# Kernel optimization log

Measured on AMD Instinct MI355X. Metric: run time of the kernel, lower is better.

The kernel has to match this reference:

```python
import jax, jax.numpy as jnp
import numpy as np

EMBED_DIM = 1152
NUM_HEADS = 16
HEAD_DIM = EMBED_DIM // NUM_HEADS  # 72
SCALE = HEAD_DIM ** -0.5


def setup_inputs() -> dict:
    key = jax.random.key(0)
    ks = jax.random.split(key, 5)
    B, S, D = 32, 729, EMBED_DIM
    hidden_states = jax.random.normal(ks[0], (B, S, D), dtype=jnp.float32)
    # fused QKV projection weight/bias (q|k|v concatenated on output dim)
    w_qkv = jax.random.normal(ks[1], (D, 3 * D), dtype=jnp.float32) * (D ** -0.5)
    b_qkv = jax.random.normal(ks[2], (3 * D,), dtype=jnp.float32) * 0.02
    w_out = jax.random.normal(ks[3], (D, D), dtype=jnp.float32) * (D ** -0.5)
    b_out = jax.random.normal(ks[4], (D,), dtype=jnp.float32) * 0.02
    return {"hidden_states": hidden_states, "w_qkv": w_qkv, "b_qkv": b_qkv,
            "w_out": w_out, "b_out": b_out}


def reference(hidden_states, w_qkv, b_qkv, w_out, b_out):
    B, S, D = hidden_states.shape
    qkv = hidden_states @ w_qkv + b_qkv              # [B,S,3D]
    q, k, v = jnp.split(qkv, 3, axis=-1)
    # [B,S,D] -> [B,H,S,hd]
    def to_heads(x):
        return x.reshape(B, S, NUM_HEADS, HEAD_DIM).transpose(0, 2, 1, 3)
    q, k, v = to_heads(q), to_heads(k), to_heads(v)
    scores = jnp.einsum('bhqd,bhkd->bhqk', q, k) * SCALE
    attn = jax.nn.softmax(scores, axis=-1)
    out = jnp.einsum('bhqk,bhkd->bhqd', attn, v)     # [B,H,S,hd]
    out = out.transpose(0, 2, 1, 3).reshape(B, S, D)
    return out @ w_out + b_out
```

## Files before the change

### kernel.cpp

```cpp
#include <hip/hip_runtime.h>
#include <hip/hip_bf16.h>
#include <stdint.h>

typedef unsigned short u16;
typedef __attribute__((ext_vector_type(8))) short bf16x8;
typedef __attribute__((ext_vector_type(4))) float f32x4;
typedef __attribute__((ext_vector_type(4))) unsigned short us4;

#define T_TOK   23328
#define MPAD    23424
#define DMODEL  1152
#define N3      3456
#define NHEAD   16
#define HDIM    72
#define SEQ     729
#define VSTR    736
#define SCALE_F 0.1178511301977579f
#define KVB     64
#define NT      12
#define THR     8.0f

__device__ __forceinline__ u16 f2bf(float f) {
  unsigned u = __builtin_bit_cast(unsigned, f);
  u += 0x7fffu + ((u >> 16) & 1u);
  return (u16)(u >> 16);
}

__device__ __forceinline__ f32x4 mfma16(bf16x8 a, bf16x8 b, f32x4 c) {
  return __builtin_amdgcn_mfma_f32_16x16x32_bf16(a, b, c, 0, 0, 0);
}

#define GL16(g, l)                                                        \
  __builtin_amdgcn_global_load_lds(                                       \
      (const __attribute__((address_space(1))) void*)(g),                 \
      (__attribute__((address_space(3))) void*)(l), 16, 0, 0)


__global__ void k_cvt_hidden(const float* __restrict__ in, u16* __restrict__ out) {
  size_t i4 = ((size_t)blockIdx.x * blockDim.x + threadIdx.x) * 4;
  if (i4 >= (size_t)MPAD * DMODEL) return;
  us4 o;
  if (i4 < (size_t)T_TOK * DMODEL) {
    float4 v = *(const float4*)(in + i4);
    o[0] = f2bf(v.x); o[1] = f2bf(v.y); o[2] = f2bf(v.z); o[3] = f2bf(v.w);
  } else {
    o[0] = 0; o[1] = 0; o[2] = 0; o[3] = 0;
  }
  *(us4*)(out + i4) = o;
}

template <int R, int C>
__global__ void k_transpose(const float* __restrict__ w, u16* __restrict__ wt) {
  size_t i = (size_t)blockIdx.x * blockDim.x + threadIdx.x;
  if (i >= (size_t)R * C) return;
  int n  = (int)(i / R);
  int kk = (int)(i - (size_t)n * R);
  wt[i] = f2bf(w[(size_t)kk * C + n]);
}

template <int EPI, int GX>
__global__ __launch_bounds__(256) void k_gemm(
    const u16* __restrict__ A, const u16* __restrict__ Bt,
    const float* __restrict__ bias,
    u16* __restrict__ qo, u16* __restrict__ ko, u16* __restrict__ vTo,
    float* __restrict__ outp)
{
  __shared__ u16 As[2][4096];
  __shared__ u16 Bs[2][4096];
  const int tid  = threadIdx.x;
  const int wave = tid >> 6;
  const int lane = tid & 63;

  constexpr int nwg = GX * 183;
  constexpr int q8 = nwg >> 3, r8 = nwg & 7;
  const int bid = blockIdx.x;
  const int xcd = bid & 7, idx = bid >> 3;
  const int wgid = (xcd < r8 ? xcd * (q8 + 1) : r8 * (q8 + 1) + (xcd - r8) * q8) + idx;
  const int m0 = (wgid / GX) * 128;
  const int n0 = (wgid % GX) * 128;

  const int wm = (wave >> 1) * 64;
  const int wn = (wave & 1) * 64;

  const int rofs = wave * 16 + (lane >> 2);
  const int cofs = (lane & 3) * 8;
  const u16* gA0 = A  + (size_t)(m0 + rofs) * DMODEL + cofs;
  const u16* gA1 = gA0 + (size_t)64 * DMODEL;
  const u16* gB0 = Bt + (size_t)(n0 + rofs) * DMODEL + cofs;
  const u16* gB1 = gB0 + (size_t)64 * DMODEL;

  const int fr = lane & 15;
  const int fk = (lane >> 4) * 8;

  auto stage = [&](int kt, int b) {
    char* a_ = (char*)As + b * 8192 + wave * 1024;
    char* b_ = (char*)Bs + b * 8192 + wave * 1024;
    GL16(gA0 + kt, a_);
    GL16(gA1 + kt, a_ + 4096);
    GL16(gB0 + kt, b_);
    GL16(gB1 + kt, b_ + 4096);
  };

  f32x4 acc[4][4] = {};

  stage(0, 0);

  int buf = 0;
  for (int kt = 0; kt < DMODEL; kt += 32) {
    if (kt + 32 < DMODEL) {
      stage(kt + 32, buf ^ 1);
      asm volatile("s_waitcnt vmcnt(4)\n\ts_barrier" ::: "memory");
    } else {
      asm volatile("s_waitcnt vmcnt(0)\n\ts_barrier" ::: "memory");
    }
    bf16x8 af[4], bfrag[4];
#pragma unroll
    for (int i = 0; i < 4; ++i)
      af[i] = *(const bf16x8*)&As[buf][(wm + i * 16 + fr) * 32 + fk];
#pragma unroll
    for (int j = 0; j < 4; ++j)
      bfrag[j] = *(const bf16x8*)&Bs[buf][(wn + j * 16 + fr) * 32 + fk];
#pragma unroll
    for (int i = 0; i < 4; ++i)
#pragma unroll
      for (int j = 0; j < 4; ++j)
        acc[i][j] = mfma16(af[i], bfrag[j], acc[i][j]);
    asm volatile("s_barrier" ::: "memory");
    buf ^= 1;
  }

#pragma unroll
  for (int j = 0; j < 4; ++j) {
    const int n = n0 + wn + j * 16 + fr;
    const float bi = bias[n];
    if (EPI == 0) {
      const int which = n / DMODEL;
      const int rr = n - which * DMODEL;
      const int h = rr / HDIM;
      const int d = rr - h * HDIM;
#pragma unroll
      for (int i = 0; i < 4; ++i) {
        const int tr = m0 + wm + i * 16 + (lane >> 4) * 4;
#pragma unroll
        for (int rg = 0; rg < 4; ++rg) {
          const int t = tr + rg;
          if (t < T_TOK) {
            const int bb = t / SEQ;
            const int s  = t - bb * SEQ;
            const int bh = bb * NHEAD + h;
            const float val = acc[i][j][rg] + bi;
            if (which == 0)
              qo[((size_t)bh * SEQ + s) * HDIM + d] = f2bf(val * SCALE_F);
            else if (which == 1)
              ko[((size_t)bh * SEQ + s) * HDIM + d] = f2bf(val);
            else
              vTo[((size_t)bh * HDIM + d) * VSTR + s] = f2bf(val);
          }
        }
      }
    } else {
#pragma unroll
      for (int i = 0; i < 4; ++i) {
        const int tr = m0 + wm + i * 16 + (lane >> 4) * 4;
#pragma unroll
        for (int rg = 0; rg < 4; ++rg) {
          const int t = tr + rg;
          if (t < T_TOK)
            outp[(size_t)t * DMODEL + n] = acc[i][j][rg] + bi;
        }
      }
    }
  }
}


__device__ __forceinline__ void stage_kv(const u16* __restrict__ kb, const u16* __restrict__ vb,
                                         u16* KsB, u16* VsB, int kt, int wv, int lane) {
#pragma unroll
  for (int rdi = 0; rdi < 2; ++rdi) {
    const int c0 = rdi * 256 + wv * 64;
    {
      const int c = c0 + lane;
      const int row = c / 9;
      const int off = (c - row * 9) * 8;
      GL16(kb + (size_t)(kt + row) * HDIM + off, KsB + (size_t)c0 * 8);
    }
    {
      const int c = c0 + lane;
      const int d = c >> 3;
      int off = kt + (((c & 7) ^ (d & 7)) << 3);
      off = off > (VSTR - 8) ? (VSTR - 8) : off;
      GL16(vb + (size_t)d * VSTR + off, VsB + (size_t)c0 * 8);
    }
  }
  if (wv == 0) {
    const int c = 512 + lane;
    const int row = c / 9;
    const int off = (c - row * 9) * 8;
    GL16(kb + (size_t)(kt + row) * HDIM + off, KsB + (size_t)512 * 8);
    const int d = c >> 3;
    int voff = kt + (((c & 7) ^ (d & 7)) << 3);
    voff = voff > (VSTR - 8) ? (VSTR - 8) : voff;
    GL16(vb + (size_t)d * VSTR + voff, VsB + (size_t)512 * 8);
  }
}

__global__ __launch_bounds__(256) void k_attn(
    const u16* __restrict__ q, const u16* __restrict__ k,
    const u16* __restrict__ vT, u16* __restrict__ aout)
{
  __shared__ alignas(16) u16 Ks[2][4640];
  __shared__ alignas(16) u16 Vs[2][5120];
  __shared__ alignas(16) u16 pl[4][16][72];

  const int tid  = threadIdx.x;
  const int wv   = tid >> 6;
  const int lane = tid & 63;
  const int fr = lane & 15;
  const int fg = lane >> 4;
  const int fk = fg * 8;

  const int bh = blockIdx.y;
  const int qbase = blockIdx.x * 64 + wv * 16;

  const u16* qb = q  + (size_t)bh * (SEQ * HDIM);
  const u16* kb = k  + (size_t)bh * (SEQ * HDIM);
  const u16* vb = vT + (size_t)bh * (HDIM * VSTR);

  if (tid < 64) { Vs[0][4608 + tid] = 0x3F80; Vs[1][4608 + tid] = 0x3F80; }
  for (int i = tid; i < 448; i += 256) { Vs[0][4672 + i] = 0; Vs[1][4672 + i] = 0; }
  if (tid < 32) { Ks[0][4608 + tid] = 0; Ks[1][4608 + tid] = 0; }

  const int qrow = qbase + fr;
  bf16x8 qf0 = {}, qf1 = {}, qf2 = {};
  if (qrow < SEQ) {
    const u16* qp = qb + (size_t)qrow * HDIM;
    qf0 = *(const bf16x8*)(qp + fk);
    qf1 = *(const bf16x8*)(qp + 32 + fk);
    if (fg == 0) qf2 = *(const bf16x8*)(qp + 64);
  }

  f32x4 oacc[5] = {};
  float mrun[4] = {-1e30f, -1e30f, -1e30f, -1e30f};

  stage_kv(kb, vb, Ks[0], Vs[0], 0, wv, lane);
  __syncthreads();

  int buf = 0;
  for (int t = 0; t < NT; ++t) {
    const int kt = t * KVB;
    if (t + 1 < NT)
      stage_kv(kb, vb, Ks[buf ^ 1], Vs[buf ^ 1], kt + KVB, wv, lane);

    const char* kB = (const char*)Ks[buf];
    f32x4 sc[4];
#pragma unroll
    for (int hh = 0; hh < 4; ++hh) {
      const char* krow = kB + (hh * 16 + fr) * 144;
      bf16x8 kf0 = *(const bf16x8*)(krow + fg * 16);
      bf16x8 kf1 = *(const bf16x8*)(krow + 64 + fg * 16);
      bf16x8 kf2 = *(const bf16x8*)(krow + 128 + fg * 16);
      f32x4 z = {};
      z = mfma16(qf0, kf0, z);
      z = mfma16(qf1, kf1, z);
      z = mfma16(qf2, kf2, z);
      sc[hh] = z;
    }
    if (kt + KVB > SEQ) {
#pragma unroll
      for (int hh = 0; hh < 4; ++hh)
        if (kt + hh * 16 + fr >= SEQ) {
          sc[hh][0] = -1e30f; sc[hh][1] = -1e30f; sc[hh][2] = -1e30f; sc[hh][3] = -1e30f;
        }
    }

    float tmx[4];
    bool needs = false;
#pragma unroll
    for (int r = 0; r < 4; ++r) {
      tmx[r] = fmaxf(fmaxf(sc[0][r], sc[1][r]), fmaxf(sc[2][r], sc[3][r]));
      needs |= (tmx[r] > mrun[r] + THR);
    }
    if (__any(needs)) {
#pragma unroll
      for (int r = 0; r < 4; ++r) {
        float tm = tmx[r];
        tm = fmaxf(tm, __shfl_xor(tm, 1));
        tm = fmaxf(tm, __shfl_xor(tm, 2));
        tm = fmaxf(tm, __shfl_xor(tm, 4));
        tm = fmaxf(tm, __shfl_xor(tm, 8));
        const float mnew = fmaxf(mrun[r], tm);
        const float resc = __expf(mrun[r] - mnew);
        mrun[r] = mnew;
#pragma unroll
        for (int v = 0; v < 5; ++v) oacc[v][r] *= resc;
      }
    }
#pragma unroll
    for (int r = 0; r < 4; ++r) {
      const int prow = fg * 4 + r;
#pragma unroll
      for (int hh = 0; hh < 4; ++hh)
        pl[wv][prow][hh * 16 + fr] = f2bf(__expf(sc[hh][r] - mrun[r]));
    }

    const bf16x8 pa0 = *(const bf16x8*)&pl[wv][fr][fk];
    const bf16x8 pa1 = *(const bf16x8*)&pl[wv][fr][32 + fk];
    const char* vB = (const char*)Vs[buf];
    const int swz = (fr & 7) << 4;
#pragma unroll
    for (int v = 0; v < 5; ++v) {
      const char* vrow = vB + (size_t)(v * 16 + fr) * 128;
      bf16x8 vf0 = *(const bf16x8*)(vrow + ((fg * 16) ^ swz));
      bf16x8 vf1 = *(const bf16x8*)(vrow + (((4 + fg) * 16) ^ swz));
      oacc[v] = mfma16(pa0, vf0, oacc[v]);
      oacc[v] = mfma16(pa1, vf1, oacc[v]);
    }

    __syncthreads();
    buf ^= 1;
  }

  const int bb = bh >> 4, h = bh & 15;
#pragma unroll
  for (int r = 0; r < 4; ++r) {
    const int row = qbase + fg * 4 + r;
    if (row < SEQ) {
      const float l = __shfl(oacc[4][r], (lane & 48) | 8);
      const float inv = 1.0f / l;
      u16* op = aout + (size_t)(bb * SEQ + row) * DMODEL + h * HDIM;
#pragma unroll
      for (int v = 0; v < 5; ++v) {
        const int d = v * 16 + fr;
        if (d < HDIM) op[d] = f2bf(oacc[v][r] * inv);
      }
    }
  }
}

extern "C" void kernel_launch(void* const* d_in, const int* in_sizes, int n_in,
                              void* d_out, int out_size, void* d_ws, size_t ws_size,
                              hipStream_t stream) {
  (void)in_sizes; (void)n_in; (void)out_size; (void)ws_size;
  const float* hs   = (const float*)d_in[0];
  const float* wqkv = (const float*)d_in[1];
  const float* bqkv = (const float*)d_in[2];
  const float* wout = (const float*)d_in[3];
  const float* bout = (const float*)d_in[4];
  float* out = (float*)d_out;

  u16* hbuf  = (u16*)d_ws;
  u16* wqkvT = hbuf  + (size_t)MPAD * DMODEL;
  u16* woutT = wqkvT + (size_t)N3 * DMODEL;
  u16* qb    = woutT + (size_t)DMODEL * DMODEL;
  u16* kb    = qb    + (size_t)512 * SEQ * HDIM;
  u16* vTb   = kb    + (size_t)512 * SEQ * HDIM;

  k_cvt_hidden<<<(MPAD * DMODEL / 4 + 255) / 256, 256, 0, stream>>>(hs, hbuf);
  k_transpose<DMODEL, N3><<<((size_t)DMODEL * N3 + 255) / 256, 256, 0, stream>>>(wqkv, wqkvT);
  k_transpose<DMODEL, DMODEL><<<((size_t)DMODEL * DMODEL + 255) / 256, 256, 0, stream>>>(wout, woutT);
  k_gemm<0, 27><<<27 * 183, 256, 0, stream>>>(hbuf, wqkvT, bqkv, qb, kb, vTb, nullptr);
  k_attn<<<dim3(12, 512), 256, 0, stream>>>(qb, kb, vTb, hbuf);
  k_gemm<1, 9><<<9 * 183, 256, 0, stream>>>(hbuf, woutT, bout, nullptr, nullptr, nullptr, out);
}
```

Before: 887.7 us.

## Use 256x256 tiled QKV GEMM with 8 waves, swizzled LDS and deeper K-step

Replaces the QKV projection GEMM with a dedicated kernel that uses 256x256 output tiles, 512 threads, 64-wide K steps, XOR-swizzled LDS layout and setprio around MFMA bursts. The weight matrix is padded to 3584 columns and the hidden buffer to 23552 rows so the grid divides evenly. The larger tile raises arithmetic intensity and reduces global traffic for the dominant GEMM. In exchange it raises register and LDS pressure, runs at one block per CU, and spends some work on the padded columns. The output GEMM is split into its own template with the M tile count adjusted.

After: 982.2 us. 10.6% more time.

```diff
diff --git a/kernel.cpp b/kernel.cpp
--- a/kernel.cpp
+++ b/kernel.cpp
@@ -8,9 +8,11 @@
 typedef __attribute__((ext_vector_type(4))) unsigned short us4;
 
 #define T_TOK   23328
-#define MPAD    23424
+#define MPAD    23552
 #define DMODEL  1152
 #define N3      3456
+#define N3P     3584
+#define NKT     18
 #define NHEAD   16
 #define HDIM    72
 #define SEQ     729
@@ -58,96 +60,123 @@
   wt[i] = f2bf(w[(size_t)kk * C + n]);
 }
 
-template <int EPI, int GX>
-__global__ __launch_bounds__(256) void k_gemm(
+template <int RIN, int CIN, int CPAD>
+__global__ void k_transpose_pad(const float* __restrict__ w, u16* __restrict__ wt) {
+  size_t i = (size_t)blockIdx.x * blockDim.x + threadIdx.x;
+  if (i >= (size_t)CPAD * RIN) return;
+  int n  = (int)(i / RIN);
+  int kk = (int)(i - (size_t)n * RIN);
+  wt[i] = (n < CIN) ? f2bf(w[(size_t)kk * CIN + n]) : (u16)0;
+}
+
+__global__ __launch_bounds__(512, 1) void k_gemm_qkv(
     const u16* __restrict__ A, const u16* __restrict__ Bt,
     const float* __restrict__ bias,
-    u16* __restrict__ qo, u16* __restrict__ ko, u16* __restrict__ vTo,
-    float* __restrict__ outp)
+    u16* __restrict__ qo, u16* __restrict__ ko, u16* __restrict__ vTo)
 {
-  __shared__ u16 As[2][4096];
-  __shared__ u16 Bs[2][4096];
+  __shared__ u16 As[2 * 2 * 128 * 64];
+  __shared__ u16 Bs[2 * 2 * 128 * 64];
   const int tid  = threadIdx.x;
-  const int wave = tid >> 6;
+  const int wv   = tid >> 6;
   const int lane = tid & 63;
-
-  constexpr int nwg = GX * 183;
-  constexpr int q8 = nwg >> 3, r8 = nwg & 7;
+  const int wr = wv >> 2;
+  const int wc = wv & 3;
+  const int fr = lane & 15;
+  const int fg = lane >> 4;
+
   const int bid = blockIdx.x;
-  const int xcd = bid & 7, idx = bid >> 3;
-  const int wgid = (xcd < r8 ? xcd * (q8 + 1) : r8 * (q8 + 1) + (xcd - r8) * q8) + idx;
-  const int m0 = (wgid / GX) * 128;
-  const int n0 = (wgid % GX) * 128;
-
-  const int wm = (wave >> 1) * 64;
-  const int wn = (wave & 1) * 64;
-
-  const int rofs = wave * 16 + (lane >> 2);
-  const int cofs = (lane & 3) * 8;
-  const u16* gA0 = A  + (size_t)(m0 + rofs) * DMODEL + cofs;
-  const u16* gA1 = gA0 + (size_t)64 * DMODEL;
-  const u16* gB0 = Bt + (size_t)(n0 + rofs) * DMODEL + cofs;
-  const u16* gB1 = gB0 + (size_t)64 * DMODEL;
-
-  const int fr = lane & 15;
-  const int fk = (lane >> 4) * 8;
-
-  auto stage = [&](int kt, int b) {
-    char* a_ = (char*)As + b * 8192 + wave * 1024;
-    char* b_ = (char*)Bs + b * 8192 + wave * 1024;
-    GL16(gA0 + kt, a_);
-    GL16(gA1 + kt, a_ + 4096);
-    GL16(gB0 + kt, b_);
-    GL16(gB1 + kt, b_ + 4096);
+  const int wgid = (bid & 7) * 161 + (bid >> 3);
+  const int m0 = (wgid / 14) * 256;
+  const int n0 = (wgid % 14) * 256;
+
+  int r_[2], e_[2];
+#pragma unroll
+  for (int j = 0; j < 2; ++j) {
+    const int d  = (j * 512 + wv * 64 + lane) * 16;
+    const int dd = d ^ (((d >> 9) & 1) << 5);
+    r_[j] = dd >> 7;
+    e_[j] = (dd & 127) >> 1;
+  }
+
+  auto stage_tile = [&](int t2) {
+    const int p2 = t2 & 1;
+    char* ab = (char*)As + p2 * 32768;
+    char* bb = (char*)Bs + p2 * 32768;
+    const int kt = t2 * 64;
+#pragma unroll
+    for (int h = 0; h < 2; ++h)
+#pragma unroll
+      for (int j = 0; j < 2; ++j)
+        GL16(A + (size_t)(m0 + h * 128 + r_[j]) * DMODEL + kt + e_[j],
+             ab + h * 16384 + j * 8192 + wv * 1024);
+#pragma unroll
+    for (int h = 0; h < 2; ++h)
+#pragma unroll
+      for (int j = 0; j < 2; ++j)
+        GL16(Bt + (size_t)(n0 + h * 128 + r_[j]) * DMODEL + kt + e_[j],
+             bb + h * 16384 + j * 8192 + wv * 1024);
   };
 
-  f32x4 acc[4][4] = {};
-
-  stage(0, 0);
-
-  int buf = 0;
-  for (int kt = 0; kt < DMODEL; kt += 32) {
-    if (kt + 32 < DMODEL) {
-      stage(kt + 32, buf ^ 1);
-      asm volatile("s_waitcnt vmcnt(4)\n\ts_barrier" ::: "memory");
+  const int aswz = ((fr >> 2) & 1) << 5;
+  const int kof[2] = { (fg * 16) ^ aswz, (64 + fg * 16) ^ aswz };
+  const int arow = fr * 128;
+  const int brow = ((wc & 1) * 64 + fr) * 128;
+
+  f32x4 acc[8][4] = {};
+
+  stage_tile(0);
+  stage_tile(1);
+  asm volatile("s_waitcnt vmcnt(8)\n\ts_barrier" ::: "memory");
+
+  for (int t = 0; t < NKT; ++t) {
+    const int p = t & 1;
+    const char* aB = (const char*)As + p * 32768 + wr * 16384;
+    const char* bB = (const char*)Bs + p * 32768 + (wc >> 1) * 16384;
+    __builtin_amdgcn_s_setprio(1);
+#pragma unroll
+    for (int ks = 0; ks < 2; ++ks) {
+      bf16x8 af[8], bf[4];
+#pragma unroll
+      for (int i = 0; i < 8; ++i)
+        af[i] = *(const bf16x8*)(aB + arow + i * 2048 + kof[ks]);
+#pragma unroll
+      for (int j = 0; j < 4; ++j)
+        bf[j] = *(const bf16x8*)(bB + brow + j * 2048 + kof[ks]);
+#pragma unroll
+      for (int i = 0; i < 8; ++i)
+#pragma unroll
+        for (int j = 0; j < 4; ++j)
+          acc[i][j] = mfma16(af[i], bf[j], acc[i][j]);
+    }
+    __builtin_amdgcn_s_setprio(0);
+    asm volatile("s_waitcnt lgkmcnt(0)\n\ts_barrier" ::: "memory");
+    if (t + 2 < NKT) {
+      stage_tile(t + 2);
+      asm volatile("s_waitcnt vmcnt(8)\n\ts_barrier" ::: "memory");
     } else {
       asm volatile("s_waitcnt vmcnt(0)\n\ts_barrier" ::: "memory");
     }
-    bf16x8 af[4], bfrag[4];
-#pragma unroll
-    for (int i = 0; i < 4; ++i)
-      af[i] = *(const bf16x8*)&As[buf][(wm + i * 16 + fr) * 32 + fk];
-#pragma unroll
-    for (int j = 0; j < 4; ++j)
-      bfrag[j] = *(const bf16x8*)&Bs[buf][(wn + j * 16 + fr) * 32 + fk];
-#pragma unroll
-    for (int i = 0; i < 4; ++i)
-#pragma unroll
-      for (int j = 0; j < 4; ++j)
-        acc[i][j] = mfma16(af[i], bfrag[j], acc[i][j]);
-    asm volatile("s_barrier" ::: "memory");
-    buf ^= 1;
   }
 
 #pragma unroll
   for (int j = 0; j < 4; ++j) {
-    const int n = n0 + wn + j * 16 + fr;
-    const float bi = bias[n];
-    if (EPI == 0) {
+    const int n = n0 + wc * 64 + j * 16 + fr;
+    if (n < N3) {
+      const float bi = bias[n];
       const int which = n / DMODEL;
       const int rr = n - which * DMODEL;
       const int h = rr / HDIM;
       const int d = rr - h * HDIM;
 #pragma unroll
-      for (int i = 0; i < 4; ++i) {
-        const int tr = m0 + wm + i * 16 + (lane >> 4) * 4;
+      for (int i = 0; i < 8; ++i) {
+        const int tr = m0 + wr * 128 + i * 16 + (lane >> 4) * 4;
 #pragma unroll
         for (int rg = 0; rg < 4; ++rg) {
           const int t = tr + rg;
           if (t < T_TOK) {
-            const int bb = t / SEQ;
-            const int s  = t - bb * SEQ;
-            const int bh = bb * NHEAD + h;
+            const int bb2 = t / SEQ;
+            const int s   = t - bb2 * SEQ;
+            const int bh  = bb2 * NHEAD + h;
             const float val = acc[i][j][rg] + bi;
             if (which == 0)
               qo[((size_t)bh * SEQ + s) * HDIM + d] = f2bf(val * SCALE_F);
@@ -158,16 +187,91 @@
           }
         }
       }
+    }
+  }
+}
+
+template <int GX, int MT>
+__global__ __launch_bounds__(256) void k_gemm_out(
+    const u16* __restrict__ A, const u16* __restrict__ Bt,
+    const float* __restrict__ bias, float* __restrict__ outp)
+{
+  __shared__ u16 As[2][4096];
+  __shared__ u16 Bs[2][4096];
+  const int tid  = threadIdx.x;
+  const int wave = tid >> 6;
+  const int lane = tid & 63;
+
+  constexpr int nwg = GX * MT;
+  constexpr int q8 = nwg >> 3, r8 = nwg & 7;
+  const int bid = blockIdx.x;
+  const int xcd = bid & 7, idx = bid >> 3;
+  const int wgid = (xcd < r8 ? xcd * (q8 + 1) : r8 * (q8 + 1) + (xcd - r8) * q8) + idx;
+  const int m0 = (wgid / GX) * 128;
+  const int n0 = (wgid % GX) * 128;
+
+  const int wm = (wave >> 1) * 64;
+  const int wn = (wave & 1) * 64;
+
+  const int rofs = wave * 16 + (lane >> 2);
+  const int cofs = (lane & 3) * 8;
+  const u16* gA0 = A  + (size_t)(m0 + rofs) * DMODEL + cofs;
+  const u16* gA1 = gA0 + (size_t)64 * DMODEL;
+  const u16* gB0 = Bt + (size_t)(n0 + rofs) * DMODEL + cofs;
+  const u16* gB1 = gB0 + (size_t)64 * DMODEL;
+
+  const int fr = lane & 15;
+  const int fk = (lane >> 4) * 8;
+
+  auto stage = [&](int kt, int b) {
+    char* a_ = (char*)As + b * 8192 + wave * 1024;
+    char* b_ = (char*)Bs + b * 8192 + wave * 1024;
+    GL16(gA0 + kt, a_);
+    GL16(gA1 + kt, a_ + 4096);
+    GL16(gB0 + kt, b_);
+    GL16(gB1 + kt, b_ + 4096);
+  };
+
+  f32x4 acc[4][4] = {};
+
+  stage(0, 0);
+
+  int buf = 0;
+  for (int kt = 0; kt < DMODEL; kt += 32) {
+    if (kt + 32 < DMODEL) {
+      stage(kt + 32, buf ^ 1);
+      asm volatile("s_waitcnt vmcnt(4)\n\ts_barrier" ::: "memory");
     } else {
-#pragma unroll
-      for (int i = 0; i < 4; ++i) {
-        const int tr = m0 + wm + i * 16 + (lane >> 4) * 4;
-#pragma unroll
-        for (int rg = 0; rg < 4; ++rg) {
-          const int t = tr + rg;
-          if (t < T_TOK)
-            outp[(size_t)t * DMODEL + n] = acc[i][j][rg] + bi;
-        }
+      asm volatile("s_waitcnt vmcnt(0)\n\ts_barrier" ::: "memory");
+    }
+    bf16x8 af[4], bfrag[4];
+#pragma unroll
+    for (int i = 0; i < 4; ++i)
+      af[i] = *(const bf16x8*)&As[buf][(wm + i * 16 + fr) * 32 + fk];
+#pragma unroll
+    for (int j = 0; j < 4; ++j)
+      bfrag[j] = *(const bf16x8*)&Bs[buf][(wn + j * 16 + fr) * 32 + fk];
+#pragma unroll
+    for (int i = 0; i < 4; ++i)
+#pragma unroll
+      for (int j = 0; j < 4; ++j)
+        acc[i][j] = mfma16(af[i], bfrag[j], acc[i][j]);
+    asm volatile("s_barrier" ::: "memory");
+    buf ^= 1;
+  }
+
+#pragma unroll
+  for (int j = 0; j < 4; ++j) {
+    const int n = n0 + wn + j * 16 + fr;
+    const float bi = bias[n];
+#pragma unroll
+    for (int i = 0; i < 4; ++i) {
+      const int tr = m0 + wm + i * 16 + (lane >> 4) * 4;
+#pragma unroll
+      for (int rg = 0; rg < 4; ++rg) {
+        const int t = tr + rg;
+        if (t < T_TOK)
+          outp[(size_t)t * DMODEL + n] = acc[i][j][rg] + bi;
       }
     }
   }
@@ -351,15 +455,15 @@
 
   u16* hbuf  = (u16*)d_ws;
   u16* wqkvT = hbuf  + (size_t)MPAD * DMODEL;
-  u16* woutT = wqkvT + (size_t)N3 * DMODEL;
+  u16* woutT = wqkvT + (size_t)N3P * DMODEL;
   u16* qb    = woutT + (size_t)DMODEL * DMODEL;
   u16* kb    = qb    + (size_t)512 * SEQ * HDIM;
   u16* vTb   = kb    + (size_t)512 * SEQ * HDIM;
 
-  k_cvt_hidden<<<(MPAD * DMODEL / 4 + 255) / 256, 256, 0, stream>>>(hs, hbuf);
-  k_transpose<DMODEL, N3><<<((size_t)DMODEL * N3 + 255) / 256, 256, 0, stream>>>(wqkv, wqkvT);
+  k_cvt_hidden<<<((size_t)MPAD * DMODEL / 4 + 255) / 256, 256, 0, stream>>>(hs, hbuf);
+  k_transpose_pad<DMODEL, N3, N3P><<<((size_t)N3P * DMODEL + 255) / 256, 256, 0, stream>>>(wqkv, wqkvT);
   k_transpose<DMODEL, DMODEL><<<((size_t)DMODEL * DMODEL + 255) / 256, 256, 0, stream>>>(wout, woutT);
-  k_gemm<0, 27><<<27 * 183, 256, 0, stream>>>(hbuf, wqkvT, bqkv, qb, kb, vTb, nullptr);
+  k_gemm_qkv<<<92 * 14, 512, 0, stream>>>(hbuf, wqkvT, bqkv, qb, kb, vTb);
   k_attn<<<dim3(12, 512), 256, 0, stream>>>(qb, kb, vTb, hbuf);
-  k_gemm<1, 9><<<9 * 183, 256, 0, stream>>>(hbuf, woutT, bout, nullptr, nullptr, nullptr, out);
-}
+  k_gemm_out<9, 184><<<9 * 184, 256, 0, stream>>>(hbuf, woutT, bout, out);
+}
```
